# Optimization experiments

Measured on AMD Instinct MI355X. Metric: run time of the kernel, lower is better.

## Reference

```python
import jax, jax.numpy as jnp
import numpy as np

B, T, N, U = 16, 512, 2048, 64  # batch_size, dim1, dim2 (=nodes), units


def setup_inputs() -> dict:
    key = jax.random.key(0)
    k1, k2, k3, k4 = jax.random.split(key, 4)
    x = jax.random.normal(k1, (B, T, N), dtype=jnp.float32)
    Adj = jax.random.uniform(k2, (N, N), dtype=jnp.float32)
    W = jax.random.normal(k3, (U, N), dtype=jnp.float32) * 0.05  # 'uniform' init stand-in
    b = jax.random.normal(k4, (U,), dtype=jnp.float32) * 0.05
    return {"x": x, "Adj": Adj, "W": W, "b": b}


def reference(x, Adj, W, b):
    # Original loop: out_i[b,t,j] = sum_k x[b,t,k] * Adj[j,k] * W[i,k] + b[i],
    # then mean over i. By linearity this equals a single matmul with the
    # unit-averaged weight vector and the averaged bias.
    w_bar = jnp.mean(W, axis=0)              # [N]
    w_eff = Adj * w_bar                       # [N(j), N(k)] : Adj[j,k] * w_bar[k]
    out = jnp.einsum('btk,jk->btj', x, w_eff) + jnp.mean(b)
    return out  # [B, T, N]
```

## Files before the change

### kernel.cpp

```cpp
#include <hip/hip_runtime.h>

#define N_DIM 2048
#define U_DIM 64
#define M_DIM 8192
#define K_DIM 2048

typedef __bf16 bf16x8 __attribute__((ext_vector_type(8)));
typedef float  floatx4 __attribute__((ext_vector_type(4)));
typedef unsigned short ushort8 __attribute__((ext_vector_type(8)));

#define AS1 __attribute__((address_space(1)))
#define AS3 __attribute__((address_space(3)))

__device__ __forceinline__ unsigned short f_to_bf16_rne(float f) {
    unsigned int x;
    __builtin_memcpy(&x, &f, 4);
    x += 0x7fffu + ((x >> 16) & 1u);
    return (unsigned short)(x >> 16);
}

__global__ __launch_bounds__(256) void prep_kernel(
    const float* __restrict__ W, const float* __restrict__ b,
    float* __restrict__ wbar, float* __restrict__ bmean) {
    int k = blockIdx.x * 256 + threadIdx.x;
    float s = 0.f;
#pragma unroll
    for (int i = 0; i < U_DIM; ++i) s += W[i * N_DIM + k];
    wbar[k] = s * (1.f / U_DIM);

    if (blockIdx.x == 0 && threadIdx.x < 64) {
        float v = b[threadIdx.x];
#pragma unroll
        for (int off = 32; off > 0; off >>= 1) v += __shfl_down(v, off);
        if (threadIdx.x == 0) bmean[0] = v * (1.f / U_DIM);
    }
}

__global__ __launch_bounds__(256) void weff_convx_kernel(
    const float* __restrict__ Adj, const float* __restrict__ wbar,
    unsigned short* __restrict__ weff,
    const float* __restrict__ x, unsigned short* __restrict__ xbf) {
    if (blockIdx.x < 2048) {
        long long idx = ((long long)blockIdx.x * 256 + threadIdx.x) * 8;
        int k = (int)(idx & (N_DIM - 1));
        floatx4 a0 = *(const floatx4*)(Adj + idx);
        floatx4 a1 = *(const floatx4*)(Adj + idx + 4);
        floatx4 w0 = *(const floatx4*)(wbar + k);
        floatx4 w1 = *(const floatx4*)(wbar + k + 4);
        ushort8 ov;
#pragma unroll
        for (int j = 0; j < 4; ++j) {
            ov[j]     = f_to_bf16_rne(a0[j] * w0[j]);
            ov[j + 4] = f_to_bf16_rne(a1[j] * w1[j]);
        }
        *(ushort8*)(weff + idx) = ov;
    } else {
        long long idx = ((long long)(blockIdx.x - 2048) * 256 + threadIdx.x) * 8;
        floatx4 a0 = *(const floatx4*)(x + idx);
        floatx4 a1 = *(const floatx4*)(x + idx + 4);
        ushort8 ov;
#pragma unroll
        for (int j = 0; j < 4; ++j) {
            ov[j]     = f_to_bf16_rne(a0[j]);
            ov[j + 4] = f_to_bf16_rne(a1[j]);
        }
        *(ushort8*)(xbf + idx) = ov;
    }
}

__global__ __launch_bounds__(256) void convx_kernel(
    const float* __restrict__ x, unsigned short* __restrict__ xbf) {
    long long idx = ((long long)blockIdx.x * 256 + threadIdx.x) * 8;
    floatx4 a0 = *(const floatx4*)(x + idx);
    floatx4 a1 = *(const floatx4*)(x + idx + 4);
    ushort8 ov;
#pragma unroll
    for (int j = 0; j < 4; ++j) {
        ov[j]     = f_to_bf16_rne(a0[j]);
        ov[j + 4] = f_to_bf16_rne(a1[j]);
    }
    *(ushort8*)(xbf + idx) = ov;
}

#define BM 128
#define BN 128
#define BK 64

__global__ __launch_bounds__(256) void gemm_bt_kernel(
    const unsigned short* __restrict__ A,
    const unsigned short* __restrict__ Bt,
    const float* __restrict__ bmeanp,
    float* __restrict__ C,
    int mtiles) {
    __shared__ __align__(16) unsigned short sA[BM * BK];
    __shared__ __align__(16) unsigned short sB[BN * BK];

    const int id    = blockIdx.x;
    const int xcd   = id & 7;
    const int local = id >> 3;
    const int nt    = xcd * 2 + (local & 1);
    const int mt    = local >> 1;
    const int tile_m = mt * BM;
    const int tile_n = nt * BN;

    const int tid  = threadIdx.x;
    const int w    = tid >> 6;
    const int lane = tid & 63;

    const float bmean = bmeanp[0];

    const int srow_in = lane >> 3;
    const int skc     = (lane & 7) ^ srow_in;
    const int scol    = skc * 8;
    const unsigned short* gA[4];
    const unsigned short* gB[4];
    unsigned short* lA[4];
    unsigned short* lB[4];
#pragma unroll
    for (int i = 0; i < 4; ++i) {
        int c = w * 4 + i;
        gA[i] = A  + (size_t)(tile_m + c * 8 + srow_in) * K_DIM + scol;
        gB[i] = Bt + (size_t)(tile_n + c * 8 + srow_in) * K_DIM + scol;
        lA[i] = &sA[c * 8 * BK];
        lB[i] = &sB[c * 8 * BK];
    }

    const int wrow = (w >> 1) * 64;
    const int wcol = (w & 1) * 64;
    const int fr = lane & 15;
    const int fq = lane >> 4;
    int aoff[4][2], boff[4][2];
#pragma unroll
    for (int i = 0; i < 4; ++i)
#pragma unroll
        for (int s = 0; s < 2; ++s) {
            int kc = s * 4 + fq;
            int slot = kc ^ (fr & 7);
            aoff[i][s] = (wrow + i * 16 + fr) * BK + slot * 8;
            boff[i][s] = (wcol + i * 16 + fr) * BK + slot * 8;
        }

    floatx4 acc[4][4];
#pragma unroll
    for (int mi = 0; mi < 4; ++mi)
#pragma unroll
        for (int ni = 0; ni < 4; ++ni) acc[mi][ni] = (floatx4){0.f, 0.f, 0.f, 0.f};

    for (int k0 = 0; k0 < K_DIM; k0 += BK) {
        __syncthreads();
#pragma unroll
        for (int i = 0; i < 4; ++i) {
            __builtin_amdgcn_global_load_lds((const AS1 void*)(gA[i] + k0),
                                             (AS3 void*)lA[i], 16, 0, 0);
            __builtin_amdgcn_global_load_lds((const AS1 void*)(gB[i] + k0),
                                             (AS3 void*)lB[i], 16, 0, 0);
        }
        __syncthreads();

#pragma unroll
        for (int s = 0; s < 2; ++s) {
            bf16x8 af[4], bf[4];
#pragma unroll
            for (int i = 0; i < 4; ++i) {
                af[i] = *(const bf16x8*)&sA[aoff[i][s]];
                bf[i] = *(const bf16x8*)&sB[boff[i][s]];
            }
#pragma unroll
            for (int mi = 0; mi < 4; ++mi)
#pragma unroll
                for (int ni = 0; ni < 4; ++ni)
                    acc[mi][ni] = __builtin_amdgcn_mfma_f32_16x16x32_bf16(
                        af[mi], bf[ni], acc[mi][ni], 0, 0, 0);
        }
    }

    const int crow = tile_m + wrow + fq * 4;
    const int ccol = tile_n + wcol + fr;
#pragma unroll
    for (int mi = 0; mi < 4; ++mi)
#pragma unroll
        for (int ni = 0; ni < 4; ++ni)
#pragma unroll
            for (int r = 0; r < 4; ++r) {
                int gm = crow + mi * 16 + r;
                int gn = ccol + ni * 16;
                C[(size_t)gm * N_DIM + gn] = acc[mi][ni][r] + bmean;
            }
    (void)mtiles;
}

extern "C" void kernel_launch(void* const* d_in, const int* in_sizes, int n_in,
                              void* d_out, int out_size, void* d_ws, size_t ws_size,
                              hipStream_t stream) {
    (void)in_sizes; (void)n_in; (void)out_size;
    const float* x   = (const float*)d_in[0];
    const float* Adj = (const float*)d_in[1];
    const float* W   = (const float*)d_in[2];
    const float* b   = (const float*)d_in[3];
    float* out = (float*)d_out;

    char* ws = (char*)d_ws;
    float* wbar  = (float*)ws;
    float* bmean = (float*)(ws + 8192);
    unsigned short* weff = (unsigned short*)(ws + 16384);
    const size_t weff_bytes = (size_t)N_DIM * N_DIM * 2;
    const size_t xbf_off = 16384 + weff_bytes;
    unsigned short* xbf = (unsigned short*)(ws + xbf_off);

    size_t avail = (ws_size > xbf_off) ? (ws_size - xbf_off) : 0;
    long long max_rows = (long long)(avail / ((size_t)K_DIM * 2)) / BM * BM;
    if (max_rows < BM) max_rows = BM;
    if (max_rows > M_DIM) max_rows = M_DIM;

    prep_kernel<<<N_DIM / 256, 256, 0, stream>>>(W, b, wbar, bmean);

    if (max_rows == M_DIM) {
        weff_convx_kernel<<<2048 + M_DIM, 256, 0, stream>>>(Adj, wbar, weff, x, xbf);
        gemm_bt_kernel<<<(N_DIM / BN) * (M_DIM / BM), 256, 0, stream>>>(
            xbf, weff, bmean, out, M_DIM / BM);
    } else {
        weff_convx_kernel<<<2048, 256, 0, stream>>>(Adj, wbar, weff, x, xbf);
        for (long long m0 = 0; m0 < M_DIM; m0 += max_rows) {
            long long rows = (M_DIM - m0 < max_rows) ? (M_DIM - m0) : max_rows;
            convx_kernel<<<(int)rows, 256, 0, stream>>>(x + m0 * K_DIM, xbf);
            gemm_bt_kernel<<<(N_DIM / BN) * (int)(rows / BM), 256, 0, stream>>>(
                xbf, weff, bmean, out + m0 * (size_t)N_DIM, (int)(rows / BM));
        }
    }
}
```

Measured before the change: 226.8 us.

## Enlarge GEMM tiles to 256x256 with double-buffered LDS prefetch pipeline

```diff
diff --git a/kernel.cpp b/kernel.cpp
--- a/kernel.cpp
+++ b/kernel.cpp
@@ -82,102 +82,110 @@
     *(ushort8*)(xbf + idx) = ov;
 }
 
-#define BM 128
-#define BN 128
+#define BM 256
+#define BN 256
 #define BK 64
-
-__global__ __launch_bounds__(256) void gemm_bt_kernel(
+#define NT (K_DIM / BK)
+
+__global__ __launch_bounds__(512, 2) void gemm_bt_kernel(
     const unsigned short* __restrict__ A,
     const unsigned short* __restrict__ Bt,
     const float* __restrict__ bmeanp,
     float* __restrict__ C,
     int mtiles) {
-    __shared__ __align__(16) unsigned short sA[BM * BK];
-    __shared__ __align__(16) unsigned short sB[BN * BK];
-
-    const int id    = blockIdx.x;
-    const int xcd   = id & 7;
-    const int local = id >> 3;
-    const int nt    = xcd * 2 + (local & 1);
-    const int mt    = local >> 1;
+    __shared__ __align__(16) unsigned short sA[2][BM * BK];
+    __shared__ __align__(16) unsigned short sB[2][BN * BK];
+
+    const int id   = blockIdx.x;
+    const int nt   = id & 7;
+    const int mt   = id >> 3;
     const int tile_m = mt * BM;
     const int tile_n = nt * BN;
 
     const int tid  = threadIdx.x;
     const int w    = tid >> 6;
     const int lane = tid & 63;
+    const int wm   = w >> 2;
+    const int wn   = w & 3;
 
     const float bmean = bmeanp[0];
 
-    const int srow_in = lane >> 3;
-    const int skc     = (lane & 7) ^ srow_in;
-    const int scol    = skc * 8;
-    const unsigned short* gA[4];
-    const unsigned short* gB[4];
-    unsigned short* lA[4];
-    unsigned short* lB[4];
-#pragma unroll
-    for (int i = 0; i < 4; ++i) {
-        int c = w * 4 + i;
-        gA[i] = A  + (size_t)(tile_m + c * 8 + srow_in) * K_DIM + scol;
-        gB[i] = Bt + (size_t)(tile_n + c * 8 + srow_in) * K_DIM + scol;
-        lA[i] = &sA[c * 8 * BK];
-        lB[i] = &sB[c * 8 * BK];
-    }
-
-    const int wrow = (w >> 1) * 64;
-    const int wcol = (w & 1) * 64;
+    const int srow = lane >> 3;
+    const int skc  = (lane & 7) ^ srow;
+    const unsigned short* gA0 = A  + (size_t)(tile_m + w * 32 + srow) * K_DIM + skc * 8;
+    const unsigned short* gB0 = Bt + (size_t)(tile_n + w * 32 + srow) * K_DIM + skc * 8;
+
     const int fr = lane & 15;
     const int fq = lane >> 4;
-    int aoff[4][2], boff[4][2];
-#pragma unroll
-    for (int i = 0; i < 4; ++i)
+    int aoff[2], boff[2];
+#pragma unroll
+    for (int s = 0; s < 2; ++s) {
+        int slot = ((s * 4 + fq) ^ (fr & 7)) * 8;
+        aoff[s] = (wm * 128 + fr) * BK + slot;
+        boff[s] = (wn * 64 + fr) * BK + slot;
+    }
+
+    floatx4 acc[8][4];
+#pragma unroll
+    for (int mi = 0; mi < 8; ++mi)
+#pragma unroll
+        for (int ni = 0; ni < 4; ++ni) acc[mi][ni] = (floatx4){0.f, 0.f, 0.f, 0.f};
+
+    #define STAGE(p, kt)                                                          \
+        do {                                                                      \
+            const int koff_ = (kt) * BK;                                          \
+            _Pragma("unroll")                                                     \
+            for (int i_ = 0; i_ < 4; ++i_) {                                      \
+                __builtin_amdgcn_global_load_lds(                                 \
+                    (const AS1 void*)(gA0 + koff_ + (size_t)i_ * 8 * K_DIM),      \
+                    (AS3 void*)(&sA[(p)][(w * 4 + i_) * 8 * BK]), 16, 0, 0);      \
+                __builtin_amdgcn_global_load_lds(                                 \
+                    (const AS1 void*)(gB0 + koff_ + (size_t)i_ * 8 * K_DIM),      \
+                    (AS3 void*)(&sB[(p)][(w * 4 + i_) * 8 * BK]), 16, 0, 0);      \
+            }                                                                     \
+        } while (0)
+
+    STAGE(0, 0);
+    STAGE(1, 1);
+
+    for (int t = 0; t < NT; ++t) {
+        const int p = t & 1;
+
+        if (t == NT - 1) asm volatile("s_waitcnt vmcnt(0)" ::: "memory");
+        else             asm volatile("s_waitcnt vmcnt(8)" ::: "memory");
+        __builtin_amdgcn_s_barrier();
+
 #pragma unroll
         for (int s = 0; s < 2; ++s) {
-            int kc = s * 4 + fq;
-            int slot = kc ^ (fr & 7);
-            aoff[i][s] = (wrow + i * 16 + fr) * BK + slot * 8;
-            boff[i][s] = (wcol + i * 16 + fr) * BK + slot * 8;
-        }
-
-    floatx4 acc[4][4];
-#pragma unroll
-    for (int mi = 0; mi < 4; ++mi)
-#pragma unroll
-        for (int ni = 0; ni < 4; ++ni) acc[mi][ni] = (floatx4){0.f, 0.f, 0.f, 0.f};
-
-    for (int k0 = 0; k0 < K_DIM; k0 += BK) {
-        __syncthreads();
-#pragma unroll
-        for (int i = 0; i < 4; ++i) {
-            __builtin_amdgcn_global_load_lds((const AS1 void*)(gA[i] + k0),
-                                             (AS3 void*)lA[i], 16, 0, 0);
-            __builtin_amdgcn_global_load_lds((const AS1 void*)(gB[i] + k0),
-                                             (AS3 void*)lB[i], 16, 0, 0);
-        }
-        __syncthreads();
-
-#pragma unroll
-        for (int s = 0; s < 2; ++s) {
-            bf16x8 af[4], bf[4];
-#pragma unroll
-            for (int i = 0; i < 4; ++i) {
-                af[i] = *(const bf16x8*)&sA[aoff[i][s]];
-                bf[i] = *(const bf16x8*)&sB[boff[i][s]];
-            }
-#pragma unroll
-            for (int mi = 0; mi < 4; ++mi)
+            bf16x8 af[8], bfr[4];
+#pragma unroll
+            for (int mi = 0; mi < 8; ++mi)
+                af[mi] = *(const bf16x8*)&sA[p][aoff[s] + mi * 16 * BK];
+#pragma unroll
+            for (int ni = 0; ni < 4; ++ni)
+                bfr[ni] = *(const bf16x8*)&sB[p][boff[s] + ni * 16 * BK];
+            asm volatile("s_waitcnt lgkmcnt(0)" ::: "memory");
+            __builtin_amdgcn_sched_barrier(0);
+            __builtin_amdgcn_s_setprio(1);
+#pragma unroll
+            for (int mi = 0; mi < 8; ++mi)
 #pragma unroll
                 for (int ni = 0; ni < 4; ++ni)
                     acc[mi][ni] = __builtin_amdgcn_mfma_f32_16x16x32_bf16(
-                        af[mi], bf[ni], acc[mi][ni], 0, 0, 0);
-        }
-    }
-
-    const int crow = tile_m + wrow + fq * 4;
-    const int ccol = tile_n + wcol + fr;
-#pragma unroll
-    for (int mi = 0; mi < 4; ++mi)
+                        af[mi], bfr[ni], acc[mi][ni], 0, 0, 0);
+            __builtin_amdgcn_s_setprio(0);
+        }
+
+        __builtin_amdgcn_s_barrier();
+
+        if (t + 2 < NT) STAGE(p, t + 2);
+    }
+    #undef STAGE
+
+    const int crow = tile_m + wm * 128 + fq * 4;
+    const int ccol = tile_n + wn * 64 + fr;
+#pragma unroll
+    for (int mi = 0; mi < 8; ++mi)
 #pragma unroll
         for (int ni = 0; ni < 4; ++ni)
 #pragma unroll
@@ -216,14 +224,14 @@
 
     if (max_rows == M_DIM) {
         weff_convx_kernel<<<2048 + M_DIM, 256, 0, stream>>>(Adj, wbar, weff, x, xbf);
-        gemm_bt_kernel<<<(N_DIM / BN) * (M_DIM / BM), 256, 0, stream>>>(
+        gemm_bt_kernel<<<(M_DIM / BM) * (N_DIM / BN), 512, 0, stream>>>(
             xbf, weff, bmean, out, M_DIM / BM);
     } else {
         weff_convx_kernel<<<2048, 256, 0, stream>>>(Adj, wbar, weff, x, xbf);
         for (long long m0 = 0; m0 < M_DIM; m0 += max_rows) {
             long long rows = (M_DIM - m0 < max_rows) ? (M_DIM - m0) : max_rows;
             convx_kernel<<<(int)rows, 256, 0, stream>>>(x + m0 * K_DIM, xbf);
-            gemm_bt_kernel<<<(N_DIM / BN) * (int)(rows / BM), 256, 0, stream>>>(
+            gemm_bt_kernel<<<(int)(rows / BM) * (N_DIM / BN), 512, 0, stream>>>(
                 xbf, weff, bmean, out + m0 * (size_t)N_DIM, (int)(rows / BM));
         }
     }
```

New measurement: 224.5 us. No clear change (-1.0%).
